# Kernel optimization log

Hardware: AMD Instinct MI355X
Metric: run time of the kernel (lower is better)

Reference implementation:

```python
import jax, jax.numpy as jnp
import numpy as np

NUM_GROUPS = 2          # ['dark_skin', 'light_skin']
NUM_SUBGROUPS = 6       # 2 skin tones x 3 classes
NUM_CLASSES = 3
BAL_ACC_W = 0.3         # GroupDROConfig.BALANCED_ACCURACY_WEIGHT
BRIGHTNESS_THRESH = 0.4 # _estimate_skin_tone_from_image threshold

N = 16777216


def setup_inputs() -> dict:
    key = jax.random.key(0)
    k1, k2 = jax.random.split(key)
    logits = jax.random.normal(k1, (N, NUM_CLASSES), dtype=jnp.float32)
    labels = jax.random.randint(k2, (N,), 0, NUM_CLASSES, dtype=jnp.int32)
    group_weights = jnp.ones((NUM_GROUPS,), dtype=jnp.float32)  # buffer init
    return {"logits": logits, "labels": labels, "group_weights": group_weights}


def reference(logits, labels, group_weights):
    # per-sample cross entropy (reduction='none')
    log_probs = jax.nn.log_softmax(logits, axis=-1)              # [N, C]
    ce = -jnp.take_along_axis(log_probs, labels[:, None], axis=-1)[:, 0]  # [N]

    # group assignment: forward passes logits as 'images'; fallback brightness
    # estimate is mean over the sample; < 0.4 -> dark (idx 0) else light (idx 1)
    brightness = jnp.mean(logits, axis=-1)                        # [N]
    group_idx = jnp.where(brightness < BRIGHTNESS_THRESH, 0, 1).astype(jnp.int32)
    subgroup_idx = group_idx * NUM_CLASSES + labels               # [N], in [0,6)

    # scatter-add (segment reduce) of per-sample CE into group / subgroup bins
    group_losses = jax.ops.segment_sum(ce, group_idx, num_segments=NUM_GROUPS)
    subgroup_losses = jax.ops.segment_sum(ce, subgroup_idx, num_segments=NUM_SUBGROUPS)

    # weighted worst-group style aggregation
    total_loss = jnp.sum(group_losses * group_weights)
    standard_loss = jnp.mean(ce)  # F.cross_entropy default mean reduction
    combined_loss = (1.0 - BAL_ACC_W) * standard_loss + BAL_ACC_W * total_loss
    return combined_loss, group_losses, subgroup_losses
```

## Files before the change

### kernel.cpp

```cpp
#include <hip/hip_runtime.h>


constexpr int N_SAMPLES = 16777216;
constexpr int BLOCK = 256;
constexpr int GRID = 2048;
constexpr int WAVES = BLOCK / 64;

__global__ __launch_bounds__(BLOCK) void dro_partial(
    const float* __restrict__ logits,
    const int*   __restrict__ labels,
    float*       __restrict__ bins)
{
    const int nq = N_SAMPLES / 4;
    const float4* __restrict__ lg = (const float4*)logits;
    const int4*   __restrict__ lb = (const int4*)labels;

    float acc[6] = {0.f, 0.f, 0.f, 0.f, 0.f, 0.f};

    for (int q = blockIdx.x * BLOCK + threadIdx.x; q < nq; q += GRID * BLOCK) {
        float4 p0 = lg[3 * q + 0];
        float4 p1 = lg[3 * q + 1];
        float4 p2 = lg[3 * q + 2];
        int4   l4 = lb[q];

        float xs[12] = {p0.x, p0.y, p0.z, p0.w, p1.x, p1.y,
                        p1.z, p1.w, p2.x, p2.y, p2.z, p2.w};
        int   ls[4]  = {l4.x, l4.y, l4.z, l4.w};

        #pragma unroll
        for (int s = 0; s < 4; ++s) {
            float a = xs[3 * s], b = xs[3 * s + 1], c = xs[3 * s + 2];
            int lab = ls[s];

            float m  = fmaxf(a, fmaxf(b, c));
            float ea = __expf(a - m), eb = __expf(b - m), ec = __expf(c - m);
            float lse = m + __logf(ea + eb + ec);
            float xl = (lab == 0) ? a : ((lab == 1) ? b : c);
            float ce = lse - xl;

            float mean = (a + b + c) * (1.0f / 3.0f);
            int g  = (mean < 0.4f) ? 0 : 1;
            int sg = g * 3 + lab;

            #pragma unroll
            for (int j = 0; j < 6; ++j)
                acc[j] += (j == sg) ? ce : 0.0f;
        }
    }

    #pragma unroll
    for (int j = 0; j < 6; ++j) {
        #pragma unroll
        for (int off = 32; off > 0; off >>= 1)
            acc[j] += __shfl_down(acc[j], off, 64);
    }

    __shared__ float lds[WAVES][6];
    int wave = threadIdx.x >> 6;
    int lane = threadIdx.x & 63;
    if (lane == 0) {
        #pragma unroll
        for (int j = 0; j < 6; ++j) lds[wave][j] = acc[j];
    }
    __syncthreads();

    if (threadIdx.x < 6) {
        float s = 0.f;
        #pragma unroll
        for (int w = 0; w < WAVES; ++w) s += lds[w][threadIdx.x];
        atomicAdd(&bins[threadIdx.x], s);
    }
}

__global__ void dro_finalize(const float* __restrict__ bins,
                             const float* __restrict__ gw,
                             float* __restrict__ out)
{
    if (threadIdx.x == 0 && blockIdx.x == 0) {
        float sg[6];
        float tot = 0.f;
        #pragma unroll
        for (int j = 0; j < 6; ++j) { sg[j] = bins[j]; tot += sg[j]; }
        float g0 = sg[0] + sg[1] + sg[2];
        float g1 = sg[3] + sg[4] + sg[5];
        float total_loss = g0 * gw[0] + g1 * gw[1];
        float standard   = tot / (float)N_SAMPLES;
        float combined   = 0.7f * standard + 0.3f * total_loss;
        out[0] = combined;
        out[1] = g0;
        out[2] = g1;
        #pragma unroll
        for (int j = 0; j < 6; ++j) out[3 + j] = sg[j];
    }
}

extern "C" void kernel_launch(void* const* d_in, const int* in_sizes, int n_in,
                              void* d_out, int out_size, void* d_ws, size_t ws_size,
                              hipStream_t stream) {
    const float* logits = (const float*)d_in[0];
    const int*   labels = (const int*)d_in[1];
    const float* gw     = (const float*)d_in[2];
    float* bins = (float*)d_ws;
    float* out  = (float*)d_out;

    hipMemsetAsync(bins, 0, 6 * sizeof(float), stream);
    dro_partial<<<GRID, BLOCK, 0, stream>>>(logits, labels, bins);
    dro_finalize<<<1, 64, 0, stream>>>(bins, gw, out);
}
```

Before: 323.4 us.

## Replace global atomics with per-block partials and a parallel finalize reduction

Each block now writes its six subgroup sums to a workspace slot, and the finalize kernel reduces all slots with a full block instead of using atomics. This also drops the memset launch. The grid is halved and the loop becomes a fixed-trip-count loop unrolled by two so more loads are in flight per thread. The finalize step does more work, and halving the grid could lower memory-level parallelism.

```diff
diff --git a/kernel.cpp b/kernel.cpp
--- a/kernel.cpp
+++ b/kernel.cpp
@@ -2,22 +2,29 @@
 
 
 constexpr int N_SAMPLES = 16777216;
+constexpr int NQ = N_SAMPLES / 4;
 constexpr int BLOCK = 256;
-constexpr int GRID = 2048;
+constexpr int GRID = 1024;
+constexpr int STRIDE = GRID * BLOCK;
+constexpr int ITERS = NQ / STRIDE;
 constexpr int WAVES = BLOCK / 64;
+
+static_assert(ITERS * STRIDE == NQ, "exact tiling");
 
 __global__ __launch_bounds__(BLOCK) void dro_partial(
     const float* __restrict__ logits,
     const int*   __restrict__ labels,
-    float*       __restrict__ bins)
+    float*       __restrict__ partials)
 {
-    const int nq = N_SAMPLES / 4;
     const float4* __restrict__ lg = (const float4*)logits;
     const int4*   __restrict__ lb = (const int4*)labels;
 
     float acc[6] = {0.f, 0.f, 0.f, 0.f, 0.f, 0.f};
+    const int base = blockIdx.x * BLOCK + threadIdx.x;
 
-    for (int q = blockIdx.x * BLOCK + threadIdx.x; q < nq; q += GRID * BLOCK) {
+    #pragma unroll 2
+    for (int it = 0; it < ITERS; ++it) {
+        const int q = base + it * STRIDE;
         float4 p0 = lg[3 * q + 0];
         float4 p1 = lg[3 * q + 1];
         float4 p2 = lg[3 * q + 2];
@@ -56,8 +63,8 @@
     }
 
     __shared__ float lds[WAVES][6];
-    int wave = threadIdx.x >> 6;
-    int lane = threadIdx.x & 63;
+    const int wave = threadIdx.x >> 6;
+    const int lane = threadIdx.x & 63;
     if (lane == 0) {
         #pragma unroll
         for (int j = 0; j < 6; ++j) lds[wave][j] = acc[j];
@@ -68,19 +75,48 @@
         float s = 0.f;
         #pragma unroll
         for (int w = 0; w < WAVES; ++w) s += lds[w][threadIdx.x];
-        atomicAdd(&bins[threadIdx.x], s);
+        partials[blockIdx.x * 6 + threadIdx.x] = s;
     }
 }
 
-__global__ void dro_finalize(const float* __restrict__ bins,
-                             const float* __restrict__ gw,
-                             float* __restrict__ out)
+__global__ __launch_bounds__(BLOCK) void dro_finalize(
+    const float* __restrict__ partials,
+    const float* __restrict__ gw,
+    float* __restrict__ out)
 {
-    if (threadIdx.x == 0 && blockIdx.x == 0) {
+    float acc[6] = {0.f, 0.f, 0.f, 0.f, 0.f, 0.f};
+    for (int b = threadIdx.x; b < GRID; b += BLOCK) {
+        #pragma unroll
+        for (int j = 0; j < 6; ++j) acc[j] += partials[b * 6 + j];
+    }
+
+    #pragma unroll
+    for (int j = 0; j < 6; ++j) {
+        #pragma unroll
+        for (int off = 32; off > 0; off >>= 1)
+            acc[j] += __shfl_down(acc[j], off, 64);
+    }
+
+    __shared__ float lds[WAVES][6];
+    const int wave = threadIdx.x >> 6;
+    const int lane = threadIdx.x & 63;
+    if (lane == 0) {
+        #pragma unroll
+        for (int j = 0; j < 6; ++j) lds[wave][j] = acc[j];
+    }
+    __syncthreads();
+
+    if (threadIdx.x == 0) {
         float sg[6];
         float tot = 0.f;
         #pragma unroll
-        for (int j = 0; j < 6; ++j) { sg[j] = bins[j]; tot += sg[j]; }
+        for (int j = 0; j < 6; ++j) {
+            float s = 0.f;
+            #pragma unroll
+            for (int w = 0; w < WAVES; ++w) s += lds[w][j];
+            sg[j] = s;
+            tot += s;
+        }
         float g0 = sg[0] + sg[1] + sg[2];
         float g1 = sg[3] + sg[4] + sg[5];
         float total_loss = g0 * gw[0] + g1 * gw[1];
@@ -100,10 +136,9 @@
     const float* logits = (const float*)d_in[0];
     const int*   labels = (const int*)d_in[1];
     const float* gw     = (const float*)d_in[2];
-    float* bins = (float*)d_ws;
-    float* out  = (float*)d_out;
+    float* partials = (float*)d_ws;
+    float* out      = (float*)d_out;
 
-    hipMemsetAsync(bins, 0, 6 * sizeof(float), stream);
-    dro_partial<<<GRID, BLOCK, 0, stream>>>(logits, labels, bins);
-    dro_finalize<<<1, 64, 0, stream>>>(bins, gw, out);
+    dro_partial<<<GRID, BLOCK, 0, stream>>>(logits, labels, partials);
+    dro_finalize<<<1, BLOCK, 0, stream>>>(partials, gw, out);
 }
```

After: 319.8 us. About the same (-1.1%).
